# Performance work log

Hardware: AMD Instinct MI355X
Metric: run time of the kernel (lower is better)

The kernel has to match this reference:

```python
import jax, jax.numpy as jnp
import numpy as np
import math

NUM_HEADS = 8


def _skew(QEr):
    # QEr: (B, H, S, S). Music-Transformer skew: pad one col on the left,
    # reshape (S, S+1) -> (S+1, S), drop first row -> relative scores Srel.
    B, H, S, _ = QEr.shape
    padded = jnp.pad(QEr, ((0, 0), (0, 0), (0, 0), (1, 0)))  # (B,H,S,S+1)
    reshaped = padded.reshape(B, H, S + 1, S)
    return reshaped[:, :, 1:, :]  # (B,H,S,S)


def setup_inputs() -> dict:
    key = jax.random.key(0)
    ks = jax.random.split(key, 8)
    B, S, D = 4, 2048, 512
    dh = D // NUM_HEADS
    scale = 0.02
    return {
        "x": jax.random.normal(ks[0], (B, S, D), jnp.float32),
        "Wq": jax.random.normal(ks[1], (D, D), jnp.float32) * scale,
        "bq": jnp.zeros((D,), jnp.float32),
        "Wk": jax.random.normal(ks[2], (D, D), jnp.float32) * scale,
        "bk": jnp.zeros((D,), jnp.float32),
        "Wv": jax.random.normal(ks[3], (D, D), jnp.float32) * scale,
        "bv": jnp.zeros((D,), jnp.float32),
        "Er": jax.random.normal(ks[4], (S, dh), jnp.float32),  # max_len == S
    }


def reference(x, Wq, bq, Wk, bk, Wv, bv, Er):
    B, S, D = x.shape
    H = NUM_HEADS
    dh = D // H
    # torch Linear: y = x @ W.T + b
    q = (x @ Wq.T + bq).reshape(B, S, H, dh).transpose(0, 2, 1, 3)  # (B,H,S,dh)
    k = (x @ Wk.T + bk).reshape(B, S, H, dh).transpose(0, 2, 1, 3)
    v = (x @ Wv.T + bv).reshape(B, S, H, dh).transpose(0, 2, 1, 3)
    # relative position scores; start = max_len - seq_len = 0 here
    max_len = Er.shape[0]
    Er_used = Er[max_len - S:, :]  # (S, dh)
    QEr = jnp.einsum("bhsd,rd->bhsr", q, Er_used)  # (B,H,S,S)
    Srel = _skew(QEr)
    scores = (jnp.einsum("bhsd,bhtd->bhst", q, k) + Srel) / math.sqrt(dh)
    causal = jnp.tril(jnp.ones((S, S), bool))
    scores = jnp.where(causal, scores, -jnp.inf)
    attn = jax.nn.softmax(scores, axis=-1)
    out = jnp.einsum("bhst,bhtd->bhsd", attn, v)  # (B,H,S,dh)
    return out.transpose(0, 2, 1, 3).reshape(B, S, D)
```

## Files before the change

kernel.cpp:

```cpp
#include <hip/hip_runtime.h>
#include <hip/hip_bf16.h>

#define S_LEN 2048
#define NHEADS 8
#define DHEAD 64
#define NBATCH 4
#define DMODEL 512

typedef __attribute__((ext_vector_type(8))) short short8;
typedef __attribute__((ext_vector_type(4))) short short4v;
typedef __attribute__((ext_vector_type(4))) float f32x4;

__device__ __forceinline__ short f2bf(float f) {
    unsigned int u = __builtin_bit_cast(unsigned int, f);
    u = (u + 0x7fffu + ((u >> 16) & 1u)) >> 16;
    return (short)u;
}

__global__ __launch_bounds__(256) void conv_bf16(
    const float* __restrict__ x, const float* __restrict__ Wq,
    const float* __restrict__ Wk, const float* __restrict__ Wv,
    const float* __restrict__ er,
    unsigned short* __restrict__ xb, unsigned short* __restrict__ wb,
    unsigned short* __restrict__ erb)
{
    const int bid = blockIdx.x;
    const float* src;
    unsigned short* dst;
    int idx;
    if (bid < 4096) {
        src = x; dst = xb; idx = bid * 256 + threadIdx.x;
    } else if (bid < 4864) {
        const int m = (bid - 4096) >> 8;
        src = (m == 0) ? Wq : (m == 1) ? Wk : Wv;
        dst = wb + m * (DMODEL * DMODEL);
        idx = ((bid - 4096) & 255) * 256 + threadIdx.x;
    } else {
        src = er; dst = erb;
        idx = (bid - 4864) * 256 + threadIdx.x;
    }
    float4 v = *(const float4*)(src + idx * 4);
    short4v s;
    s[0] = f2bf(v.x); s[1] = f2bf(v.y); s[2] = f2bf(v.z); s[3] = f2bf(v.w);
    *(short4v*)(dst + idx * 4) = s;
}

__global__ __launch_bounds__(256) void qkv_gemm(
    const unsigned short* __restrict__ xb,
    const unsigned short* __restrict__ wb,
    const float* __restrict__ bq, const float* __restrict__ bk,
    const float* __restrict__ bv,
    unsigned short* __restrict__ qkv)
{
    __shared__ __align__(16) short smem[64 * 136];
    short* xt = smem;
    short* wt = smem + 128 * 40;
    const int tid = threadIdx.x;
    const int w = tid >> 6;
    const int l = tid & 63;
    const int lrow = l & 15, lgrp = l >> 4;
    const int m0 = blockIdx.x * 128;
    const int nb = blockIdx.y;
    const int mat = nb >> 3, hh = nb & 7;
    const unsigned short* wmat = wb + mat * (DMODEL * DMODEL);
    const float* bias = (mat == 0) ? bq : ((mat == 1) ? bk : bv);
    const int n0 = hh * 64;

    f32x4 acc[2][4];
    #pragma unroll
    for (int i = 0; i < 2; i++)
        #pragma unroll
        for (int j = 0; j < 4; j++) acc[i][j] = (f32x4)0.0f;

    const int xur = tid >> 2, xus = tid & 3;
    const int wur = tid >> 2, wus = tid & 3;

    for (int k0 = 0; k0 < DMODEL; k0 += 32) {
        short8 xa0 = *(const short8*)(xb + (size_t)(m0 + xur) * DMODEL + k0 + xus * 8);
        short8 xa1 = *(const short8*)(xb + (size_t)(m0 + xur + 64) * DMODEL + k0 + xus * 8);
        short8 wa  = *(const short8*)(wmat + (size_t)(n0 + wur) * DMODEL + k0 + wus * 8);
        *(short8*)(xt + xur * 40 + xus * 8)        = xa0;
        *(short8*)(xt + (xur + 64) * 40 + xus * 8) = xa1;
        *(short8*)(wt + wur * 40 + wus * 8)        = wa;
        __syncthreads();
        #pragma unroll
        for (int nc = 0; nc < 4; nc++) {
            short8 bfrag = *(const short8*)(wt + (nc * 16 + lrow) * 40 + lgrp * 8);
            #pragma unroll
            for (int mf = 0; mf < 2; mf++) {
                short8 afrag = *(const short8*)(xt + (w * 32 + mf * 16 + lrow) * 40 + lgrp * 8);
                acc[mf][nc] = __builtin_amdgcn_mfma_f32_16x16x32_bf16(afrag, bfrag, acc[mf][nc], 0, 0, 0);
            }
        }
        __syncthreads();
    }

    const int b  = m0 >> 11;
    const int s0 = m0 & (S_LEN - 1);
    if (mat == 2) {
        short* vl = smem;
        #pragma unroll
        for (int nc = 0; nc < 4; nc++) {
            const int d = nc * 16 + lrow;
            const float bias_v = bias[n0 + d];
            #pragma unroll
            for (int mf = 0; mf < 2; mf++)
                #pragma unroll
                for (int r = 0; r < 4; r++) {
                    const int sl = w * 32 + mf * 16 + lgrp * 4 + r;
                    vl[d * 136 + sl] = f2bf(acc[mf][nc][r] + bias_v);
                }
        }
        __syncthreads();
        unsigned short* ob = qkv + (((size_t)2 * NBATCH + b) * NHEADS + hh) * S_LEN * DHEAD;
        #pragma unroll
        for (int kch = 0; kch < 4; kch++) {
            const int c = kch * 256 + tid;
            const int d = c >> 4, seg = c & 15;
            short8 ch = *(const short8*)(vl + d * 136 + seg * 8);
            *(short8*)(ob + (size_t)d * S_LEN + s0 + seg * 8) = ch;
        }
    } else {
        const float oscale = (mat == 0) ? 0.18033688f : 1.0f;
        unsigned short* ob = qkv + (((size_t)mat * NBATCH + b) * NHEADS + hh) * S_LEN * DHEAD;
        #pragma unroll
        for (int nc = 0; nc < 4; nc++) {
            const int d = nc * 16 + lrow;
            const float bias_v = bias[n0 + d];
            #pragma unroll
            for (int mf = 0; mf < 2; mf++) {
                #pragma unroll
                for (int r = 0; r < 4; r++) {
                    int srow = s0 + w * 32 + mf * 16 + lgrp * 4 + r;
                    ob[(size_t)srow * DHEAD + d] =
                        (unsigned short)f2bf((acc[mf][nc][r] + bias_v) * oscale);
                }
            }
        }
    }
}

__global__ __launch_bounds__(256) void rga_attn(
    const unsigned short* __restrict__ qkv,
    const unsigned short* __restrict__ er,
    float* __restrict__ out)
{
    __shared__ __align__(16) unsigned short klds[2][64 * 64];
    __shared__ __align__(16) unsigned short vt[2][64 * 72];
    __shared__ __align__(16) unsigned short plds[4][16 * 64];

    const int tid = threadIdx.x;
    const int w = tid >> 6;
    const int l = tid & 63;
    const int lrow = l & 15, lgrp = l >> 4;
    const int p  = blockIdx.x;
    const int bh = blockIdx.y;
    const int b = bh >> 3, hh = bh & 7;

    const unsigned short* qp  = qkv + (size_t)bh * S_LEN * DHEAD;
    const unsigned short* kp  = qkv + ((size_t)(NBATCH * NHEADS) + bh) * S_LEN * DHEAD;
    const unsigned short* vtg = qkv + ((size_t)(2 * NBATCH * NHEADS) + bh) * S_LEN * DHEAD;

    short8 ones;
    #pragma unroll
    for (int e = 0; e < 8; e++) ones[e] = (short)0x3F80;

    const int tr0 = tid >> 3, tr1 = (tid >> 3) + 32, seg = tid & 7;
    unsigned short* pw = plds[w];

    #pragma unroll 1
    for (int sp = 0; sp < 2; sp++) {
        const int sid = sp ? p : (31 - p);
        const int q0 = sid * 64;
        const int s_base = q0 + w * 16;
        const int nt = sid + 1;

        short8 aq[2];
        {
            const unsigned short* qr = qp + (size_t)(s_base + lrow) * DHEAD + lgrp * 8;
            aq[0] = *(const short8*)(qr);
            aq[1] = *(const short8*)(qr + 32);
        }

        f32x4 o[4], lsum;
        lsum = (f32x4)0.0f;
        #pragma unroll
        for (int n = 0; n < 4; n++) o[n] = (f32x4)0.0f;

        short8 kreg[2], vreg[2], ereg0[5], ereg1[5];
        kreg[0] = *(const short8*)(kp + (size_t)tr0 * DHEAD + seg * 8);
        kreg[1] = *(const short8*)(kp + (size_t)tr1 * DHEAD + seg * 8);
        vreg[0] = *(const short8*)(vtg + (size_t)tr0 * S_LEN + seg * 8);
        vreg[1] = *(const short8*)(vtg + (size_t)tr1 * S_LEN + seg * 8);
        *(short8*)((char*)klds[0] + tr0 * 128 + ((seg * 16) ^ ((tr0 & 7) << 4))) = kreg[0];
        *(short8*)((char*)klds[0] + tr1 * 128 + ((seg * 16) ^ ((tr1 & 7) << 4))) = kreg[1];
        *(short8*)(vt[0] + tr0 * 72 + seg * 8) = vreg[0];
        *(short8*)(vt[0] + tr1 * 72 + seg * 8) = vreg[1];
        if (nt > 1) {
            kreg[0] = *(const short8*)(kp + (size_t)(64 + tr0) * DHEAD + seg * 8);
            kreg[1] = *(const short8*)(kp + (size_t)(64 + tr1) * DHEAD + seg * 8);
            vreg[0] = *(const short8*)(vtg + (size_t)tr0 * S_LEN + 64 + seg * 8);
            vreg[1] = *(const short8*)(vtg + (size_t)tr1 * S_LEN + 64 + seg * 8);
        }
        {
            const int r_lo = -s_base + (S_LEN - 16);
            #pragma unroll
            for (int f = 0; f < 5; f++) {
                int rr = r_lo + f * 16 + lrow;
                rr = rr < 0 ? 0 : (rr > (S_LEN - 1) ? (S_LEN - 1) : rr);
                const unsigned short* ep = er + (size_t)rr * DHEAD + lgrp * 8;
                ereg0[f] = *(const short8*)(ep);
                ereg1[f] = *(const short8*)(ep + 32);
            }
        }
        __syncthreads();

        for (int it = 0; it < nt; it++) {
            const int t0 = it << 6;
            const int cur = it & 1;
            if (it + 1 < nt) {
                unsigned short* kd = klds[cur ^ 1];
                unsigned short* vd = vt[cur ^ 1];
                *(short8*)((char*)kd + tr0 * 128 + ((seg * 16) ^ ((tr0 & 7) << 4))) = kreg[0];
                *(short8*)((char*)kd + tr1 * 128 + ((seg * 16) ^ ((tr1 & 7) << 4))) = kreg[1];
                *(short8*)(vd + tr0 * 72 + seg * 8) = vreg[0];
                *(short8*)(vd + tr1 * 72 + seg * 8) = vreg[1];
            }
            f32x4 qe[5];
            __builtin_amdgcn_s_setprio(1);
            #pragma unroll
            for (int f = 0; f < 5; f++) {
                f32x4 a = (f32x4)0.0f;
                a = __builtin_amdgcn_mfma_f32_16x16x32_bf16(aq[0], ereg0[f], a, 0, 0, 0);
                a = __builtin_amdgcn_mfma_f32_16x16x32_bf16(aq[1], ereg1[f], a, 0, 0, 0);
                qe[f] = a;
            }
            __builtin_amdgcn_s_setprio(0);
            if (it + 2 < nt) {
                const int tn = t0 + 128;
                kreg[0] = *(const short8*)(kp + (size_t)(tn + tr0) * DHEAD + seg * 8);
                kreg[1] = *(const short8*)(kp + (size_t)(tn + tr1) * DHEAD + seg * 8);
                vreg[0] = *(const short8*)(vtg + (size_t)tr0 * S_LEN + tn + seg * 8);
                vreg[1] = *(const short8*)(vtg + (size_t)tr1 * S_LEN + tn + seg * 8);
            }
            if (it + 1 < nt) {
                const int r_lo = t0 + 64 - s_base + (S_LEN - 16);
                if (t0 + 128 <= s_base) {
                    #pragma unroll
                    for (int f = 0; f < 5; f++) {
                        const unsigned short* ep = er + (size_t)(r_lo + f * 16 + lrow) * DHEAD + lgrp * 8;
                        ereg0[f] = *(const short8*)(ep);
                        ereg1[f] = *(const short8*)(ep + 32);
                    }
                } else {
                    #pragma unroll
                    for (int f = 0; f < 5; f++) {
                        int rr = r_lo + f * 16 + lrow;
                        rr = rr < 0 ? 0 : (rr > (S_LEN - 1) ? (S_LEN - 1) : rr);
                        const unsigned short* ep = er + (size_t)rr * DHEAD + lgrp * 8;
                        ereg0[f] = *(const short8*)(ep);
                        ereg1[f] = *(const short8*)(ep + 32);
                    }
                }
            }
            f32x4 sfr[4];
            __builtin_amdgcn_s_setprio(1);
            #pragma unroll
            for (int u = 0; u < 4; u++) {
                const int trow = u * 16 + lrow;
                const char* kb = (const char*)klds[cur] + trow * 128;
                const int swz = (trow & 7) << 4;
                short8 kb0 = *(const short8*)(kb + ((lgrp * 16) ^ swz));
                short8 kb1 = *(const short8*)(kb + ((64 + lgrp * 16) ^ swz));
                f32x4 a = (f32x4)0.0f;
                a = __builtin_amdgcn_mfma_f32_16x16x32_bf16(aq[0], kb0, a, 0, 0, 0);
                a = __builtin_amdgcn_mfma_f32_16x16x32_bf16(aq[1], kb1, a, 0, 0, 0);
                sfr[u] = a;
            }
            __builtin_amdgcn_s_setprio(0);
            if (t0 + 64 <= s_base) {
                #pragma unroll
                for (int r = 0; r < 4; r++) {
                    const int si = lgrp * 4 + r;
                    const int dd = lrow - si + 15;
                    const int srcl = (l & 48) | (dd & 15);
                    const int hi = dd >> 4;
                    float sh[5];
                    #pragma unroll
                    for (int f = 0; f < 5; f++) sh[f] = __shfl(qe[f][r], srcl);
                    const int pswz = (si & 7) << 4;
                    char* pr = (char*)pw + si * 128;
                    float pe[4];
                    #pragma unroll
                    for (int u = 0; u < 4; u++) {
                        const float rel = hi ? sh[u + 1] : sh[u];
                        float sc = sfr[u][r] + rel;
                        asm("v_exp_f32 %0, %1\ns_nop 1" : "=v"(pe[u]) : "v"(sc));
                    }
                    #pragma unroll
                    for (int h2 = 0; h2 < 2; h2++) {
                        unsigned pk;
                        asm("v_cvt_pk_bf16_f32 %0, %1, %2"
                            : "=v"(pk) : "v"(pe[h2 * 2]), "v"(pe[h2 * 2 + 1]));
                        *(unsigned short*)(pr + (((h2 * 32 + lrow) * 2) ^ pswz)) = (unsigned short)pk;
                        *(unsigned short*)(pr + (((h2 * 32 + 16 + lrow) * 2) ^ pswz)) = (unsigned short)(pk >> 16);
                    }
                }
            } else {
                #pragma unroll
                for (int r = 0; r < 4; r++) {
                    const int si = lgrp * 4 + r;
                    const int sg = s_base + si;
                    const int dd = lrow - si + 15;
                    const int srcl = (l & 48) | (dd & 15);
                    const int hi = dd >> 4;
                    float sh[5];
                    #pragma unroll
                    for (int f = 0; f < 5; f++) sh[f] = __shfl(qe[f][r], srcl);
                    const int pswz = (si & 7) << 4;
                    char* pr = (char*)pw + si * 128;
                    float pe[4];
                    #pragma unroll
                    for (int u = 0; u < 4; u++) {
                        const float rel = hi ? sh[u + 1] : sh[u];
                        float sc = sfr[u][r] + rel;
                        float ex;
                        asm("v_exp_f32 %0, %1\ns_nop 1" : "=v"(ex) : "v"(sc));
                        pe[u] = ((t0 + u * 16 + lrow) <= sg) ? ex : 0.0f;
                    }
                    #pragma unroll
                    for (int h2 = 0; h2 < 2; h2++) {
                        unsigned pk;
                        asm("v_cvt_pk_bf16_f32 %0, %1, %2"
                            : "=v"(pk) : "v"(pe[h2 * 2]), "v"(pe[h2 * 2 + 1]));
                        *(unsigned short*)(pr + (((h2 * 32 + lrow) * 2) ^ pswz)) = (unsigned short)pk;
                        *(unsigned short*)(pr + (((h2 * 32 + 16 + lrow) * 2) ^ pswz)) = (unsigned short)(pk >> 16);
                    }
                }
            }
            asm volatile("s_waitcnt lgkmcnt(0)" ::: "memory");
            __builtin_amdgcn_sched_barrier(0);
            __builtin_amdgcn_s_setprio(1);
            const int pswz2 = (lrow & 7) << 4;
            #pragma unroll
            for (int kk = 0; kk < 2; kk++) {
                short8 pa = *(const short8*)((const char*)pw + lrow * 128 +
                                             ((kk * 64 + lgrp * 16) ^ pswz2));
                lsum = __builtin_amdgcn_mfma_f32_16x16x32_bf16(pa, ones, lsum, 0, 0, 0);
                #pragma unroll
                for (int n = 0; n < 4; n++) {
                    short8 vb = *(const short8*)(vt[cur] + (n * 16 + lrow) * 72 + kk * 32 + lgrp * 8);
                    o[n] = __builtin_amdgcn_mfma_f32_16x16x32_bf16(pa, vb, o[n], 0, 0, 0);
                }
            }
            __builtin_amdgcn_s_setprio(0);
            __syncthreads();
        }

        #pragma unroll
        for (int r = 0; r < 4; r++) {
            const int sg = s_base + lgrp * 4 + r;
            const float inv = 1.0f / lsum[r];
            float* orow = out + ((size_t)b * S_LEN + sg) * DMODEL + hh * DHEAD;
            #pragma unroll
            for (int n = 0; n < 4; n++)
                orow[n * 16 + lrow] = o[n][r] * inv;
        }
    }
}

extern "C" void kernel_launch(void* const* d_in, const int* in_sizes, int n_in,
                              void* d_out, int out_size, void* d_ws, size_t ws_size,
                              hipStream_t stream) {
    const float* x  = (const float*)d_in[0];
    const float* Wq = (const float*)d_in[1];
    const float* bq = (const float*)d_in[2];
    const float* Wk = (const float*)d_in[3];
    const float* bk = (const float*)d_in[4];
    const float* Wv = (const float*)d_in[5];
    const float* bv = (const float*)d_in[6];
    const float* Er = (const float*)d_in[7];

    unsigned short* ws_qkv = (unsigned short*)d_ws;
    unsigned short* ws_er  = ws_qkv + (size_t)3 * NBATCH * NHEADS * S_LEN * DHEAD;

    unsigned short* xb = (unsigned short*)d_out;
    unsigned short* wb = xb + (size_t)NBATCH * S_LEN * DMODEL;

    conv_bf16<<<dim3(4096 + 3 * 256 + 128), dim3(256), 0, stream>>>(x, Wq, Wk, Wv, Er, xb, wb, ws_er);
    qkv_gemm<<<dim3(64, 24), dim3(256), 0, stream>>>(xb, wb, bq, bk, bv, ws_qkv);
    rga_attn<<<dim3(16, 32), dim3(256), 0, stream>>>(ws_qkv, ws_er, (float*)d_out);
}
```

Baseline: 127.2 us.

## Stage 128-key K/V tiles per barrier with inner 64-key sub-loop

Doubles the K and V tiles staged in LDS to 128 keys per iteration, with each thread loading four vectors, and processes them in two 64-key halves inside an inner loop. This halves the number of __syncthreads barriers and global-to-LDS staging rounds per query block. In exchange it roughly doubles K/V LDS usage, which can reduce occupancy, and it adds register pressure from the extra prefetch registers. Within a half, the Er prefetch and masking logic are unchanged.

```diff
diff --git a/kernel.cpp b/kernel.cpp
--- a/kernel.cpp
+++ b/kernel.cpp
@@ -145,8 +145,8 @@
     const unsigned short* __restrict__ er,
     float* __restrict__ out)
 {
-    __shared__ __align__(16) unsigned short klds[2][64 * 64];
-    __shared__ __align__(16) unsigned short vt[2][64 * 72];
+    __shared__ __align__(16) unsigned short klds[2][128 * 64];
+    __shared__ __align__(16) unsigned short vt[2][64 * 136];
     __shared__ __align__(16) unsigned short plds[4][16 * 64];
 
     const int tid = threadIdx.x;
@@ -165,7 +165,8 @@
     #pragma unroll
     for (int e = 0; e < 8; e++) ones[e] = (short)0x3F80;
 
-    const int tr0 = tid >> 3, tr1 = (tid >> 3) + 32, seg = tid & 7;
+    const int ktr = tid >> 3, kseg = tid & 7;
+    const int vdr = tid >> 4, vseg = tid & 15;
     unsigned short* pw = plds[w];
 
     #pragma unroll 1
@@ -173,7 +174,8 @@
         const int sid = sp ? p : (31 - p);
         const int q0 = sid * 64;
         const int s_base = q0 + w * 16;
-        const int nt = sid + 1;
+        const int nt64 = sid + 1;
+        const int nt = (nt64 + 1) >> 1;
 
         short8 aq[2];
         {
@@ -187,20 +189,24 @@
         #pragma unroll
         for (int n = 0; n < 4; n++) o[n] = (f32x4)0.0f;
 
-        short8 kreg[2], vreg[2], ereg0[5], ereg1[5];
-        kreg[0] = *(const short8*)(kp + (size_t)tr0 * DHEAD + seg * 8);
-        kreg[1] = *(const short8*)(kp + (size_t)tr1 * DHEAD + seg * 8);
-        vreg[0] = *(const short8*)(vtg + (size_t)tr0 * S_LEN + seg * 8);
-        vreg[1] = *(const short8*)(vtg + (size_t)tr1 * S_LEN + seg * 8);
-        *(short8*)((char*)klds[0] + tr0 * 128 + ((seg * 16) ^ ((tr0 & 7) << 4))) = kreg[0];
-        *(short8*)((char*)klds[0] + tr1 * 128 + ((seg * 16) ^ ((tr1 & 7) << 4))) = kreg[1];
-        *(short8*)(vt[0] + tr0 * 72 + seg * 8) = vreg[0];
-        *(short8*)(vt[0] + tr1 * 72 + seg * 8) = vreg[1];
+        short8 kreg[4], vreg[4], ereg0[5], ereg1[5];
+        #pragma unroll
+        for (int j = 0; j < 4; j++) {
+            kreg[j] = *(const short8*)(kp + (size_t)(ktr + 32 * j) * DHEAD + kseg * 8);
+            vreg[j] = *(const short8*)(vtg + (size_t)(vdr + 16 * j) * S_LEN + vseg * 8);
+        }
+        #pragma unroll
+        for (int j = 0; j < 4; j++) {
+            const int tr = ktr + 32 * j;
+            *(short8*)((char*)klds[0] + tr * 128 + ((kseg * 16) ^ ((tr & 7) << 4))) = kreg[j];
+            *(short8*)(vt[0] + (vdr + 16 * j) * 136 + vseg * 8) = vreg[j];
+        }
         if (nt > 1) {
-            kreg[0] = *(const short8*)(kp + (size_t)(64 + tr0) * DHEAD + seg * 8);
-            kreg[1] = *(const short8*)(kp + (size_t)(64 + tr1) * DHEAD + seg * 8);
-            vreg[0] = *(const short8*)(vtg + (size_t)tr0 * S_LEN + 64 + seg * 8);
-            vreg[1] = *(const short8*)(vtg + (size_t)tr1 * S_LEN + 64 + seg * 8);
+            #pragma unroll
+            for (int j = 0; j < 4; j++) {
+                kreg[j] = *(const short8*)(kp + (size_t)(128 + ktr + 32 * j) * DHEAD + kseg * 8);
+                vreg[j] = *(const short8*)(vtg + (size_t)(vdr + 16 * j) * S_LEN + 128 + vseg * 8);
+            }
         }
         {
             const int r_lo = -s_base + (S_LEN - 16);
@@ -216,144 +222,155 @@
         __syncthreads();
 
         for (int it = 0; it < nt; it++) {
-            const int t0 = it << 6;
+            const int t0 = it << 7;
             const int cur = it & 1;
             if (it + 1 < nt) {
                 unsigned short* kd = klds[cur ^ 1];
                 unsigned short* vd = vt[cur ^ 1];
-                *(short8*)((char*)kd + tr0 * 128 + ((seg * 16) ^ ((tr0 & 7) << 4))) = kreg[0];
-                *(short8*)((char*)kd + tr1 * 128 + ((seg * 16) ^ ((tr1 & 7) << 4))) = kreg[1];
-                *(short8*)(vd + tr0 * 72 + seg * 8) = vreg[0];
-                *(short8*)(vd + tr1 * 72 + seg * 8) = vreg[1];
-            }
-            f32x4 qe[5];
-            __builtin_amdgcn_s_setprio(1);
-            #pragma unroll
-            for (int f = 0; f < 5; f++) {
-                f32x4 a = (f32x4)0.0f;
-                a = __builtin_amdgcn_mfma_f32_16x16x32_bf16(aq[0], ereg0[f], a, 0, 0, 0);
-                a = __builtin_amdgcn_mfma_f32_16x16x32_bf16(aq[1], ereg1[f], a, 0, 0, 0);
-                qe[f] = a;
-            }
-            __builtin_amdgcn_s_setprio(0);
-            if (it + 2 < nt) {
-                const int tn = t0 + 128;
-                kreg[0] = *(const short8*)(kp + (size_t)(tn + tr0) * DHEAD + seg * 8);
-                kreg[1] = *(const short8*)(kp + (size_t)(tn + tr1) * DHEAD + seg * 8);
-                vreg[0] = *(const short8*)(vtg + (size_t)tr0 * S_LEN + tn + seg * 8);
-                vreg[1] = *(const short8*)(vtg + (size_t)tr1 * S_LEN + tn + seg * 8);
-            }
-            if (it + 1 < nt) {
-                const int r_lo = t0 + 64 - s_base + (S_LEN - 16);
-                if (t0 + 128 <= s_base) {
+                #pragma unroll
+                for (int j = 0; j < 4; j++) {
+                    const int tr = ktr + 32 * j;
+                    *(short8*)((char*)kd + tr * 128 + ((kseg * 16) ^ ((tr & 7) << 4))) = kreg[j];
+                    *(short8*)(vd + (vdr + 16 * j) * 136 + vseg * 8) = vreg[j];
+                }
+            }
+            #pragma unroll 1
+            for (int h = 0; h < 2; h++) {
+                const int i64 = it * 2 + h;
+                if (i64 >= nt64) break;
+                const int th0 = t0 + (h << 6);
+                f32x4 qe[5];
+                __builtin_amdgcn_s_setprio(1);
+                #pragma unroll
+                for (int f = 0; f < 5; f++) {
+                    f32x4 a = (f32x4)0.0f;
+                    a = __builtin_amdgcn_mfma_f32_16x16x32_bf16(aq[0], ereg0[f], a, 0, 0, 0);
+                    a = __builtin_amdgcn_mfma_f32_16x16x32_bf16(aq[1], ereg1[f], a, 0, 0, 0);
+                    qe[f] = a;
+                }
+                __builtin_amdgcn_s_setprio(0);
+                if (h == 0 && it + 2 < nt) {
+                    const int tn = t0 + 256;
                     #pragma unroll
-                    for (int f = 0; f < 5; f++) {
-                        const unsigned short* ep = er + (size_t)(r_lo + f * 16 + lrow) * DHEAD + lgrp * 8;
-                        ereg0[f] = *(const short8*)(ep);
-                        ereg1[f] = *(const short8*)(ep + 32);
+                    for (int j = 0; j < 4; j++) {
+                        kreg[j] = *(const short8*)(kp + (size_t)(tn + ktr + 32 * j) * DHEAD + kseg * 8);
+                        vreg[j] = *(const short8*)(vtg + (size_t)(vdr + 16 * j) * S_LEN + tn + vseg * 8);
+                    }
+                }
+                if (i64 + 1 < nt64) {
+                    const int thn = th0 + 64;
+                    const int r_lo = thn - s_base + (S_LEN - 16);
+                    if (thn + 64 <= s_base) {
+                        #pragma unroll
+                        for (int f = 0; f < 5; f++) {
+                            const unsigned short* ep = er + (size_t)(r_lo + f * 16 + lrow) * DHEAD + lgrp * 8;
+                            ereg0[f] = *(const short8*)(ep);
+                            ereg1[f] = *(const short8*)(ep + 32);
+                        }
+                    } else {
+                        #pragma unroll
+                        for (int f = 0; f < 5; f++) {
+                            int rr = r_lo + f * 16 + lrow;
+                            rr = rr < 0 ? 0 : (rr > (S_LEN - 1) ? (S_LEN - 1) : rr);
+                            const unsigned short* ep = er + (size_t)rr * DHEAD + lgrp * 8;
+                            ereg0[f] = *(const short8*)(ep);
+                            ereg1[f] = *(const short8*)(ep + 32);
+                        }
+                    }
+                }
+                f32x4 sfr[4];
+                __builtin_amdgcn_s_setprio(1);
+                #pragma unroll
+                for (int u = 0; u < 4; u++) {
+                    const int trow = (h << 6) + u * 16 + lrow;
+                    const char* kb = (const char*)klds[cur] + trow * 128;
+                    const int swz = (trow & 7) << 4;
+                    short8 kb0 = *(const short8*)(kb + ((lgrp * 16) ^ swz));
+                    short8 kb1 = *(const short8*)(kb + ((64 + lgrp * 16) ^ swz));
+                    f32x4 a = (f32x4)0.0f;
+                    a = __builtin_amdgcn_mfma_f32_16x16x32_bf16(aq[0], kb0, a, 0, 0, 0);
+                    a = __builtin_amdgcn_mfma_f32_16x16x32_bf16(aq[1], kb1, a, 0, 0, 0);
+                    sfr[u] = a;
+                }
+                __builtin_amdgcn_s_setprio(0);
+                if (th0 + 64 <= s_base) {
+                    #pragma unroll
+                    for (int r = 0; r < 4; r++) {
+                        const int si = lgrp * 4 + r;
+                        const int dd = lrow - si + 15;
+                        const int srcl = (l & 48) | (dd & 15);
+                        const int hi = dd >> 4;
+                        float sh[5];
+                        #pragma unroll
+                        for (int f = 0; f < 5; f++) sh[f] = __shfl(qe[f][r], srcl);
+                        const int pswz = (si & 7) << 4;
+                        char* pr = (char*)pw + si * 128;
+                        float pe[4];
+                        #pragma unroll
+                        for (int u = 0; u < 4; u++) {
+                            const float rel = hi ? sh[u + 1] : sh[u];
+                            float sc = sfr[u][r] + rel;
+                            asm("v_exp_f32 %0, %1\ns_nop 1" : "=v"(pe[u]) : "v"(sc));
+                        }
+                        #pragma unroll
+                        for (int h2 = 0; h2 < 2; h2++) {
+                            unsigned pk;
+                            asm("v_cvt_pk_bf16_f32 %0, %1, %2"
+                                : "=v"(pk) : "v"(pe[h2 * 2]), "v"(pe[h2 * 2 + 1]));
+                            *(unsigned short*)(pr + (((h2 * 32 + lrow) * 2) ^ pswz)) = (unsigned short)pk;
+                            *(unsigned short*)(pr + (((h2 * 32 + 16 + lrow) * 2) ^ pswz)) = (unsigned short)(pk >> 16);
+                        }
                     }
                 } else {
                     #pragma unroll
-                    for (int f = 0; f < 5; f++) {
-                        int rr = r_lo + f * 16 + lrow;
-                        rr = rr < 0 ? 0 : (rr > (S_LEN - 1) ? (S_LEN - 1) : rr);
-                        const unsigned short* ep = er + (size_t)rr * DHEAD + lgrp * 8;
-                        ereg0[f] = *(const short8*)(ep);
-                        ereg1[f] = *(const short8*)(ep + 32);
+                    for (int r = 0; r < 4; r++) {
+                        const int si = lgrp * 4 + r;
+                        const int sg = s_base + si;
+                        const int dd = lrow - si + 15;
+                        const int srcl = (l & 48) | (dd & 15);
+                        const int hi = dd >> 4;
+                        float sh[5];
+                        #pragma unroll
+                        for (int f = 0; f < 5; f++) sh[f] = __shfl(qe[f][r], srcl);
+                        const int pswz = (si & 7) << 4;
+                        char* pr = (char*)pw + si * 128;
+                        float pe[4];
+                        #pragma unroll
+                        for (int u = 0; u < 4; u++) {
+                            const float rel = hi ? sh[u + 1] : sh[u];
+                            float sc = sfr[u][r] + rel;
+                            float ex;
+                            asm("v_exp_f32 %0, %1\ns_nop 1" : "=v"(ex) : "v"(sc));
+                            pe[u] = ((th0 + u * 16 + lrow) <= sg) ? ex : 0.0f;
+                        }
+                        #pragma unroll
+                        for (int h2 = 0; h2 < 2; h2++) {
+                            unsigned pk;
+                            asm("v_cvt_pk_bf16_f32 %0, %1, %2"
+                                : "=v"(pk) : "v"(pe[h2 * 2]), "v"(pe[h2 * 2 + 1]));
+                            *(unsigned short*)(pr + (((h2 * 32 + lrow) * 2) ^ pswz)) = (unsigned short)pk;
+                            *(unsigned short*)(pr + (((h2 * 32 + 16 + lrow) * 2) ^ pswz)) = (unsigned short)(pk >> 16);
+                        }
                     }
                 }
-            }
-            f32x4 sfr[4];
-            __builtin_amdgcn_s_setprio(1);
-            #pragma unroll
-            for (int u = 0; u < 4; u++) {
-                const int trow = u * 16 + lrow;
-                const char* kb = (const char*)klds[cur] + trow * 128;
-                const int swz = (trow & 7) << 4;
-                short8 kb0 = *(const short8*)(kb + ((lgrp * 16) ^ swz));
-                short8 kb1 = *(const short8*)(kb + ((64 + lgrp * 16) ^ swz));
-                f32x4 a = (f32x4)0.0f;
-                a = __builtin_amdgcn_mfma_f32_16x16x32_bf16(aq[0], kb0, a, 0, 0, 0);
-                a = __builtin_amdgcn_mfma_f32_16x16x32_bf16(aq[1], kb1, a, 0, 0, 0);
-                sfr[u] = a;
-            }
-            __builtin_amdgcn_s_setprio(0);
-            if (t0 + 64 <= s_base) {
-                #pragma unroll
-                for (int r = 0; r < 4; r++) {
-                    const int si = lgrp * 4 + r;
-                    const int dd = lrow - si + 15;
-                    const int srcl = (l & 48) | (dd & 15);
-                    const int hi = dd >> 4;
-                    float sh[5];
+                asm volatile("s_waitcnt lgkmcnt(0)" ::: "memory");
+                __builtin_amdgcn_sched_barrier(0);
+                __builtin_amdgcn_s_setprio(1);
+                const int pswz2 = (lrow & 7) << 4;
+                #pragma unroll
+                for (int kk = 0; kk < 2; kk++) {
+                    short8 pa = *(const short8*)((const char*)pw + lrow * 128 +
+                                                 ((kk * 64 + lgrp * 16) ^ pswz2));
+                    lsum = __builtin_amdgcn_mfma_f32_16x16x32_bf16(pa, ones, lsum, 0, 0, 0);
                     #pragma unroll
-                    for (int f = 0; f < 5; f++) sh[f] = __shfl(qe[f][r], srcl);
-                    const int pswz = (si & 7) << 4;
-                    char* pr = (char*)pw + si * 128;
-                    float pe[4];
-                    #pragma unroll
-                    for (int u = 0; u < 4; u++) {
-                        const float rel = hi ? sh[u + 1] : sh[u];
-                        float sc = sfr[u][r] + rel;
-                        asm("v_exp_f32 %0, %1\ns_nop 1" : "=v"(pe[u]) : "v"(sc));
+                    for (int n = 0; n < 4; n++) {
+                        short8 vb = *(const short8*)(vt[cur] + (n * 16 + lrow) * 136 +
+                                                     (h << 6) + kk * 32 + lgrp * 8);
+                        o[n] = __builtin_amdgcn_mfma_f32_16x16x32_bf16(pa, vb, o[n], 0, 0, 0);
                     }
-                    #pragma unroll
-                    for (int h2 = 0; h2 < 2; h2++) {
-                        unsigned pk;
-                        asm("v_cvt_pk_bf16_f32 %0, %1, %2"
-                            : "=v"(pk) : "v"(pe[h2 * 2]), "v"(pe[h2 * 2 + 1]));
-                        *(unsigned short*)(pr + (((h2 * 32 + lrow) * 2) ^ pswz)) = (unsigned short)pk;
-                        *(unsigned short*)(pr + (((h2 * 32 + 16 + lrow) * 2) ^ pswz)) = (unsigned short)(pk >> 16);
-                    }
-                }
-            } else {
-                #pragma unroll
-                for (int r = 0; r < 4; r++) {
-                    const int si = lgrp * 4 + r;
-                    const int sg = s_base + si;
-                    const int dd = lrow - si + 15;
-                    const int srcl = (l & 48) | (dd & 15);
-                    const int hi = dd >> 4;
-                    float sh[5];
-                    #pragma unroll
-                    for (int f = 0; f < 5; f++) sh[f] = __shfl(qe[f][r], srcl);
-                    const int pswz = (si & 7) << 4;
-                    char* pr = (char*)pw + si * 128;
-                    float pe[4];
-                    #pragma unroll
-                    for (int u = 0; u < 4; u++) {
-                        const float rel = hi ? sh[u + 1] : sh[u];
-                        float sc = sfr[u][r] + rel;
-                        float ex;
-                        asm("v_exp_f32 %0, %1\ns_nop 1" : "=v"(ex) : "v"(sc));
-                        pe[u] = ((t0 + u * 16 + lrow) <= sg) ? ex : 0.0f;
-                    }
-                    #pragma unroll
-                    for (int h2 = 0; h2 < 2; h2++) {
-                        unsigned pk;
-                        asm("v_cvt_pk_bf16_f32 %0, %1, %2"
-                            : "=v"(pk) : "v"(pe[h2 * 2]), "v"(pe[h2 * 2 + 1]));
-                        *(unsigned short*)(pr + (((h2 * 32 + lrow) * 2) ^ pswz)) = (unsigned short)pk;
-                        *(unsigned short*)(pr + (((h2 * 32 + 16 + lrow) * 2) ^ pswz)) = (unsigned short)(pk >> 16);
-                    }
-                }
-            }
-            asm volatile("s_waitcnt lgkmcnt(0)" ::: "memory");
-            __builtin_amdgcn_sched_barrier(0);
-            __builtin_amdgcn_s_setprio(1);
-            const int pswz2 = (lrow & 7) << 4;
-            #pragma unroll
-            for (int kk = 0; kk < 2; kk++) {
-                short8 pa = *(const short8*)((const char*)pw + lrow * 128 +
-                                             ((kk * 64 + lgrp * 16) ^ pswz2));
-                lsum = __builtin_amdgcn_mfma_f32_16x16x32_bf16(pa, ones, lsum, 0, 0, 0);
-                #pragma unroll
-                for (int n = 0; n < 4; n++) {
-                    short8 vb = *(const short8*)(vt[cur] + (n * 16 + lrow) * 72 + kk * 32 + lgrp * 8);
-                    o[n] = __builtin_amdgcn_mfma_f32_16x16x32_bf16(pa, vb, o[n], 0, 0, 0);
-                }
-            }
-            __builtin_amdgcn_s_setprio(0);
+                }
+                __builtin_amdgcn_s_setprio(0);
+            }
             __syncthreads();
         }
 
```

Result: slower. 206.5 us (+62.3%).
